# Optimization experiments

Measured on AMD Instinct MI355X. Metric: run time of the kernel, lower is better.

The kernel has to match this reference:

```python
import jax, jax.numpy as jnp
import numpy as np

B, T, C, H = 2, 2048, 1024, 16
HD = C // H
EPS = 1e-5


def _gelu_tanh(x):
    # 0.5*x*(1+tanh(sqrt(2/pi)*(x+0.044715*x^3)))
    c = jnp.sqrt(jnp.asarray(2.0 / np.pi, dtype=x.dtype))
    return 0.5 * x * (1.0 + jnp.tanh(c * (x + 0.044715 * x * x * x)))


def _layernorm(x, g, b):
    mu = jnp.mean(x, axis=-1, keepdims=True)
    var = jnp.mean(jnp.square(x - mu), axis=-1, keepdims=True)
    return (x - mu) * jax.lax.rsqrt(var + EPS) * g + b


def setup_inputs() -> dict:
    key = jax.random.key(0)
    ks = jax.random.split(key, 8)
    s = lambda fan_in: 1.0 / np.sqrt(fan_in)
    return {
        "x": jax.random.normal(ks[0], (B, T, C), jnp.float32),
        "ln1_g": jnp.ones((C,), jnp.float32),
        "ln1_b": jnp.zeros((C,), jnp.float32),
        "W_attn": jax.random.normal(ks[1], (C, 3 * C), jnp.float32) * s(C),
        "b_attn": jnp.zeros((3 * C,), jnp.float32),
        "W_proj": jax.random.normal(ks[2], (C, C), jnp.float32) * s(C),
        "b_proj": jnp.zeros((C,), jnp.float32),
        "ln2_g": jnp.ones((C,), jnp.float32),
        "ln2_b": jnp.zeros((C,), jnp.float32),
        "W_fc": jax.random.normal(ks[3], (C, 4 * C), jnp.float32) * s(C),
        "b_fc": jnp.zeros((4 * C,), jnp.float32),
        "W_fc2": jax.random.normal(ks[4], (4 * C, C), jnp.float32) * s(4 * C),
        "b_fc2": jnp.zeros((C,), jnp.float32),
    }


def reference(x, ln1_g, ln1_b, W_attn, b_attn, W_proj, b_proj,
              ln2_g, ln2_b, W_fc, b_fc, W_fc2, b_fc2):
    # --- attention branch (pre-LN) ---
    h = _layernorm(x, ln1_g, ln1_b)
    qkv = h @ W_attn + b_attn                      # [B,T,3C]
    q, k, v = jnp.split(qkv, 3, axis=2)
    q = q.reshape(B, T, H, HD).transpose(0, 2, 1, 3)  # [B,H,T,HD]
    k = k.reshape(B, T, H, HD).transpose(0, 2, 1, 3)
    v = v.reshape(B, T, H, HD).transpose(0, 2, 1, 3)
    att = jnp.einsum('bhqd,bhkd->bhqk', q, k) / jnp.sqrt(jnp.asarray(HD, x.dtype))
    causal = jnp.tril(jnp.ones((T, T), bool))
    att = jnp.where(causal, att, jnp.asarray(-jnp.inf, att.dtype))
    att = jax.nn.softmax(att, axis=-1)
    y = jnp.einsum('bhqk,bhkd->bhqd', att, v)      # [B,H,T,HD]
    y = y.transpose(0, 2, 1, 3).reshape(B, T, C)
    x = x + (y @ W_proj + b_proj)
    # --- MLP branch (pre-LN) ---
    h = _layernorm(x, ln2_g, ln2_b)
    h = _gelu_tanh(h @ W_fc + b_fc)
    x = x + (h @ W_fc2 + b_fc2)
    return x
```

## Files before the change

### kernel.cpp

```cpp
#include <hip/hip_runtime.h>
#include <hip/hip_bf16.h>
#include <cstdint>
#include <cstddef>

#define B_  2
#define T_  2048
#define C_  1024
#define H_  16
#define HD_ 64
#define M_TOT 4096

typedef __bf16 bf16x8 __attribute__((ext_vector_type(8)));
typedef float  f32x4  __attribute__((ext_vector_type(4)));
typedef unsigned short u16;

__device__ __forceinline__ u16 f2bf(float f) {
  __hip_bfloat16 h = __float2bfloat16(f);
  return __builtin_bit_cast(u16, h);
}

__device__ __forceinline__ void async_cp16(const u16* g, u16* l) {
  __builtin_amdgcn_global_load_lds(
      (const __attribute__((address_space(1))) void*)g,
      (__attribute__((address_space(3))) void*)l, 16, 0, 0);
}

__device__ __forceinline__ float gelu_f(float x) {
  const float z = 0.7978845608028654f * (x + 0.044715f * x * x * x);
  return x / (1.0f + __expf(-2.0f * z));
}

__global__ __launch_bounds__(256) void ln_bf16_kernel(
    const float* __restrict__ x, const float* __restrict__ g,
    const float* __restrict__ b, u16* __restrict__ out) {
  const int row = blockIdx.x;
  const int tid = threadIdx.x;
  const float4 v = reinterpret_cast<const float4*>(x)[row * 256 + tid];
  float s  = v.x + v.y + v.z + v.w;
  float sq = v.x * v.x + v.y * v.y + v.z * v.z + v.w * v.w;
#pragma unroll
  for (int off = 32; off > 0; off >>= 1) {
    s  += __shfl_xor(s, off);
    sq += __shfl_xor(sq, off);
  }
  __shared__ float red[8];
  const int wave = tid >> 6;
  if ((tid & 63) == 0) { red[wave] = s; red[4 + wave] = sq; }
  __syncthreads();
  s  = red[0] + red[1] + red[2] + red[3];
  sq = red[4] + red[5] + red[6] + red[7];
  const float mu   = s * (1.0f / 1024.0f);
  const float rstd = rsqrtf(sq * (1.0f / 1024.0f) - mu * mu + 1e-5f);
  const float4 gv = reinterpret_cast<const float4*>(g)[tid];
  const float4 bv = reinterpret_cast<const float4*>(b)[tid];
  ushort4 o;
  o.x = f2bf((v.x - mu) * rstd * gv.x + bv.x);
  o.y = f2bf((v.y - mu) * rstd * gv.y + bv.y);
  o.z = f2bf((v.z - mu) * rstd * gv.z + bv.z);
  o.w = f2bf((v.w - mu) * rstd * gv.w + bv.w);
  reinterpret_cast<ushort4*>(out)[row * 256 + tid] = o;
}

__global__ __launch_bounds__(256) void transpose_bf16_kernel(
    const float* __restrict__ W, u16* __restrict__ Wt, int K, int N) {
  __shared__ float tile[32][33];
  const int n0 = blockIdx.x * 32, k0 = blockIdx.y * 32;
  const int tx = threadIdx.x & 31;
  const int ty = threadIdx.x >> 5;
#pragma unroll
  for (int i = 0; i < 4; ++i)
    tile[ty + 8 * i][tx] = W[(k0 + ty + 8 * i) * (size_t)N + n0 + tx];
  __syncthreads();
#pragma unroll
  for (int i = 0; i < 4; ++i)
    Wt[(n0 + ty + 8 * i) * (size_t)K + k0 + tx] = f2bf(tile[tx][ty + 8 * i]);
}

template <int MODE, int BM>
__global__ __launch_bounds__(256, 2) void gemm_kernel(
    const u16* __restrict__ A, const u16* __restrict__ Bt,
    const float* __restrict__ bias, const float* __restrict__ resid,
    float* __restrict__ outf, u16* __restrict__ outb,
    u16* __restrict__ qo, u16* __restrict__ ko, u16* __restrict__ vto,
    int M, int N, int K) {
  constexpr int MT = BM / 32;
  __shared__ __align__(16) u16 As[BM * 32];
  __shared__ __align__(16) u16 Bs[128 * 32];
  const int tid  = threadIdx.x;
  const int wave = tid >> 6, lane = tid & 63;
  const int col  = lane & 15, quad = lane >> 4;
  const int wm   = wave >> 1, wn = wave & 1;
  const int bn = blockIdx.x, bm = blockIdx.y;

  const int ar = bm * BM + wave * (BM / 4) + (lane >> 2);
  const int br = bn * 128 + wave * 32 + (lane >> 2);
  const int kc = (lane & 3) * 8;
  const u16* ap = A  + (size_t)ar * K + kc;
  const u16* bp = Bt + (size_t)br * K + kc;
  u16* as_dst = As + wave * (BM / 4) * 32;
  u16* bs_dst = Bs + wave * 1024;

  f32x4 acc[MT][4] = {};

  for (int k0 = 0; k0 < K; k0 += 32) {
    __syncthreads();
    async_cp16(ap + k0, as_dst);
    if constexpr (BM == 128) async_cp16(ap + 16 * K + k0, as_dst + 512);
    async_cp16(bp + k0,          bs_dst);
    async_cp16(bp + 16 * K + k0, bs_dst + 512);
    __syncthreads();
    bf16x8 af[MT], bf[4];
#pragma unroll
    for (int mt = 0; mt < MT; ++mt)
      af[mt] = *reinterpret_cast<const bf16x8*>(&As[(wm * (BM / 2) + mt * 16 + col) * 32 + quad * 8]);
#pragma unroll
    for (int nt = 0; nt < 4; ++nt)
      bf[nt] = *reinterpret_cast<const bf16x8*>(&Bs[(wn * 64 + nt * 16 + col) * 32 + quad * 8]);
#pragma unroll
    for (int mt = 0; mt < MT; ++mt)
#pragma unroll
      for (int nt = 0; nt < 4; ++nt)
        acc[mt][nt] = __builtin_amdgcn_mfma_f32_16x16x32_bf16(af[mt], bf[nt], acc[mt][nt], 0, 0, 0);
  }

#pragma unroll
  for (int mt = 0; mt < MT; ++mt) {
#pragma unroll
    for (int r = 0; r < 4; ++r) {
      const int grow = bm * BM + wm * (BM / 2) + mt * 16 + quad * 4 + r;
#pragma unroll
      for (int nt = 0; nt < 4; ++nt) {
        const int gcol = bn * 128 + wn * 64 + nt * 16 + col;
        const float val = acc[mt][nt][r] + bias[gcol];
        if constexpr (MODE == 0) {
          outb[(size_t)grow * N + gcol] = f2bf(gelu_f(val));
        } else if constexpr (MODE == 1) {
          outf[(size_t)grow * N + gcol] = resid[(size_t)grow * N + gcol] + val;
        } else {
          const int which = gcol >> 10, c = gcol & 1023;
          const int hh = c >> 6, dd = c & 63;
          const int bb = grow >> 11, tt = grow & 2047;
          if (which == 0)
            qo[((bb * H_ + hh) * (size_t)T_ + tt) * HD_ + dd] = f2bf(val * 0.125f);
          else if (which == 1)
            ko[((bb * H_ + hh) * (size_t)T_ + tt) * HD_ + dd] = f2bf(val);
          else
            vto[((bb * H_ + hh) * (size_t)HD_ + dd) * T_ + tt] = f2bf(val);
        }
      }
    }
  }
}

#define PSTR 68
__global__ __launch_bounds__(256, 2) void attn_kernel(
    const u16* __restrict__ q, const u16* __restrict__ k,
    const u16* __restrict__ vt, u16* __restrict__ y) {
  const int bh  = blockIdx.x;
  const int qt  = (T_ / 128 - 1) - blockIdx.y;
  const int tid = threadIdx.x;
  const int wave = tid >> 6, lane = tid & 63;
  const int col = lane & 15, quad = lane >> 4;
  const int b = bh >> 4, h = bh & 15;
  const int r0w = qt * 128 + wave * 32;

  __shared__ __align__(16) u16 Klds[64 * PSTR];
  __shared__ __align__(16) u16 Vtlds[64 * PSTR];
  __shared__ __align__(16) u16 Plds[4 * 32 * PSTR];

  bf16x8 aq[2][2];
#pragma unroll
  for (int i = 0; i < 2; ++i)
#pragma unroll
    for (int j = 0; j < 2; ++j)
      aq[i][j] = *reinterpret_cast<const bf16x8*>(
          &q[((size_t)bh * T_ + r0w + i * 16 + col) * HD_ + j * 32 + quad * 8]);

  bf16x8 ones;
#pragma unroll
  for (int jj = 0; jj < 8; ++jj) ones[jj] = (__bf16)1.0f;

  f32x4 o[2][4] = {};
  f32x4 l_acc[2] = {};

  const int srow = tid >> 3, spart = tid & 7;
  u16* pw = Plds + wave * 32 * PSTR;

  for (int kb = 0; kb <= qt * 128 + 64; kb += 64) {
    __syncthreads();
    *reinterpret_cast<uint4*>(&Klds[srow * PSTR + spart * 8]) =
        *reinterpret_cast<const uint4*>(&k[((size_t)bh * T_ + kb + srow) * HD_ + spart * 8]);
    *reinterpret_cast<uint4*>(&Klds[(srow + 32) * PSTR + spart * 8]) =
        *reinterpret_cast<const uint4*>(&k[((size_t)bh * T_ + kb + srow + 32) * HD_ + spart * 8]);
    *reinterpret_cast<uint4*>(&Vtlds[srow * PSTR + spart * 8]) =
        *reinterpret_cast<const uint4*>(&vt[((size_t)bh * HD_ + srow) * T_ + kb + spart * 8]);
    *reinterpret_cast<uint4*>(&Vtlds[(srow + 32) * PSTR + spart * 8]) =
        *reinterpret_cast<const uint4*>(&vt[((size_t)bh * HD_ + srow + 32) * T_ + kb + spart * 8]);
    __syncthreads();

    if (kb > r0w + 31) continue;

    f32x4 s[2][4];
#pragma unroll
    for (int n = 0; n < 4; ++n) {
      const bf16x8 bk0 = *reinterpret_cast<const bf16x8*>(&Klds[(n * 16 + col) * PSTR + quad * 8]);
      const bf16x8 bk1 = *reinterpret_cast<const bf16x8*>(&Klds[(n * 16 + col) * PSTR + 32 + quad * 8]);
#pragma unroll
      for (int i = 0; i < 2; ++i) {
        f32x4 z = {};
        z = __builtin_amdgcn_mfma_f32_16x16x32_bf16(aq[i][0], bk0, z, 0, 0, 0);
        s[i][n] = __builtin_amdgcn_mfma_f32_16x16x32_bf16(aq[i][1], bk1, z, 0, 0, 0);
      }
    }

    const bool domask = (kb + 63 > r0w);
#pragma unroll
    for (int i = 0; i < 2; ++i) {
#pragma unroll
      for (int n = 0; n < 4; ++n) {
#pragma unroll
        for (int r = 0; r < 4; ++r) {
          float sv = s[i][n][r];
          if (domask) {
            const int key = kb + n * 16 + col;
            const int row = r0w + i * 16 + quad * 4 + r;
            sv = (key <= row) ? sv : -1e30f;
          }
          pw[(i * 16 + quad * 4 + r) * PSTR + n * 16 + col] = f2bf(__expf(sv));
        }
      }
    }
    __builtin_amdgcn_s_waitcnt(0xC07F);

    bf16x8 ap0[2], ap1[2];
#pragma unroll
    for (int i = 0; i < 2; ++i) {
      ap0[i] = *reinterpret_cast<const bf16x8*>(&pw[(i * 16 + col) * PSTR + quad * 8]);
      ap1[i] = *reinterpret_cast<const bf16x8*>(&pw[(i * 16 + col) * PSTR + 32 + quad * 8]);
      l_acc[i] = __builtin_amdgcn_mfma_f32_16x16x32_bf16(ap0[i], ones, l_acc[i], 0, 0, 0);
      l_acc[i] = __builtin_amdgcn_mfma_f32_16x16x32_bf16(ap1[i], ones, l_acc[i], 0, 0, 0);
    }
#pragma unroll
    for (int n = 0; n < 4; ++n) {
      const bf16x8 bv0 = *reinterpret_cast<const bf16x8*>(&Vtlds[(n * 16 + col) * PSTR + quad * 8]);
      const bf16x8 bv1 = *reinterpret_cast<const bf16x8*>(&Vtlds[(n * 16 + col) * PSTR + 32 + quad * 8]);
#pragma unroll
      for (int i = 0; i < 2; ++i) {
        o[i][n] = __builtin_amdgcn_mfma_f32_16x16x32_bf16(ap0[i], bv0, o[i][n], 0, 0, 0);
        o[i][n] = __builtin_amdgcn_mfma_f32_16x16x32_bf16(ap1[i], bv1, o[i][n], 0, 0, 0);
      }
    }
  }

#pragma unroll
  for (int i = 0; i < 2; ++i) {
#pragma unroll
    for (int r = 0; r < 4; ++r) {
      const int qrow = r0w + i * 16 + quad * 4 + r;
      const float inv = 1.0f / l_acc[i][r];
#pragma unroll
      for (int n = 0; n < 4; ++n)
        y[((size_t)b * T_ + qrow) * C_ + h * HD_ + n * 16 + col] = f2bf(o[i][n][r] * inv);
    }
  }
}

extern "C" void kernel_launch(void* const* d_in, const int* in_sizes, int n_in,
                              void* d_out, int out_size, void* d_ws, size_t ws_size,
                              hipStream_t stream) {
  const float* x      = (const float*)d_in[0];
  const float* ln1_g  = (const float*)d_in[1];
  const float* ln1_b  = (const float*)d_in[2];
  const float* W_attn = (const float*)d_in[3];
  const float* b_attn = (const float*)d_in[4];
  const float* W_proj = (const float*)d_in[5];
  const float* b_proj = (const float*)d_in[6];
  const float* ln2_g  = (const float*)d_in[7];
  const float* ln2_b  = (const float*)d_in[8];
  const float* W_fc   = (const float*)d_in[9];
  const float* b_fc   = (const float*)d_in[10];
  const float* W_fc2  = (const float*)d_in[11];
  const float* b_fc2  = (const float*)d_in[12];
  float* out = (float*)d_out;

  char* p = (char*)d_ws;
  auto alloc = [&](size_t bytes) {
    char* r = p;
    p += (bytes + 255) & ~(size_t)255;
    return r;
  };
  u16*   h1      = (u16*)alloc((size_t)M_TOT * C_ * 2);
  u16*   wt_attn = (u16*)alloc((size_t)3 * C_ * C_ * 2);
  u16*   wt_proj = (u16*)alloc((size_t)C_ * C_ * 2);
  u16*   wt_fc   = (u16*)alloc((size_t)4 * C_ * C_ * 2);
  u16*   wt_fc2  = (u16*)alloc((size_t)C_ * 4 * C_ * 2);
  u16*   qbuf    = (u16*)alloc((size_t)M_TOT * C_ * 2);
  u16*   kbuf    = (u16*)alloc((size_t)M_TOT * C_ * 2);
  u16*   vtbuf   = (u16*)alloc((size_t)M_TOT * C_ * 2);
  u16*   ybuf    = (u16*)alloc((size_t)M_TOT * C_ * 2);
  float* x2      = (float*)alloc((size_t)M_TOT * C_ * 4);
  u16*   h2      = (u16*)alloc((size_t)M_TOT * C_ * 2);
  u16*   act     = (u16*)alloc((size_t)M_TOT * 4 * C_ * 2);

  transpose_bf16_kernel<<<dim3(96, 32),  256, 0, stream>>>(W_attn, wt_attn, 1024, 3072);
  transpose_bf16_kernel<<<dim3(32, 32),  256, 0, stream>>>(W_proj, wt_proj, 1024, 1024);
  transpose_bf16_kernel<<<dim3(128, 32), 256, 0, stream>>>(W_fc,   wt_fc,   1024, 4096);
  transpose_bf16_kernel<<<dim3(32, 128), 256, 0, stream>>>(W_fc2,  wt_fc2,  4096, 1024);

  ln_bf16_kernel<<<M_TOT, 256, 0, stream>>>(x, ln1_g, ln1_b, h1);

  gemm_kernel<3, 128><<<dim3(24, 32), 256, 0, stream>>>(h1, wt_attn, b_attn, nullptr,
                                                        nullptr, nullptr, qbuf, kbuf, vtbuf,
                                                        4096, 3072, 1024);
  attn_kernel<<<dim3(32, 16), 256, 0, stream>>>(qbuf, kbuf, vtbuf, ybuf);

  gemm_kernel<1, 64><<<dim3(8, 64), 256, 0, stream>>>(ybuf, wt_proj, b_proj, x,
                                                      x2, nullptr, nullptr, nullptr, nullptr,
                                                      4096, 1024, 1024);
  ln_bf16_kernel<<<M_TOT, 256, 0, stream>>>(x2, ln2_g, ln2_b, h2);

  gemm_kernel<0, 128><<<dim3(32, 32), 256, 0, stream>>>(h2, wt_fc, b_fc, nullptr,
                                                        nullptr, act, nullptr, nullptr, nullptr,
                                                        4096, 4096, 1024);
  gemm_kernel<1, 64><<<dim3(8, 64), 256, 0, stream>>>(act, wt_fc2, b_fc2, x2,
                                                      out, nullptr, nullptr, nullptr, nullptr,
                                                      4096, 1024, 4096);
}
```

Measured before the change: 385.6 us.

## Halve attention query tile and register-prefetch next K/V block

The attention kernel now processes 64 query rows per block (16 per wave) instead of 128, doubling the grid and raising the launch-bounds occupancy hint to 4. It also prefetches the next K/Vt tile into registers while computing on the current LDS tile, replacing the load-then-sync pattern. The aim is more parallelism, less causal-tail imbalance and hidden global-load latency, at the cost of each K/V tile being loaded by twice as many blocks. A redundant duplicate load of kv1 remains in the code.

```diff
diff --git a/kernel.cpp b/kernel.cpp
--- a/kernel.cpp
+++ b/kernel.cpp
@@ -153,115 +153,110 @@
 }
 
 #define PSTR 68
-__global__ __launch_bounds__(256, 2) void attn_kernel(
+__global__ __launch_bounds__(256, 4) void attn_kernel(
     const u16* __restrict__ q, const u16* __restrict__ k,
     const u16* __restrict__ vt, u16* __restrict__ y) {
   const int bh  = blockIdx.x;
-  const int qt  = (T_ / 128 - 1) - blockIdx.y;
+  const int qt  = (T_ / 64 - 1) - blockIdx.y;
   const int tid = threadIdx.x;
   const int wave = tid >> 6, lane = tid & 63;
   const int col = lane & 15, quad = lane >> 4;
   const int b = bh >> 4, h = bh & 15;
-  const int r0w = qt * 128 + wave * 32;
+  const int r0w = qt * 64 + wave * 16;
 
   __shared__ __align__(16) u16 Klds[64 * PSTR];
   __shared__ __align__(16) u16 Vtlds[64 * PSTR];
-  __shared__ __align__(16) u16 Plds[4 * 32 * PSTR];
-
-  bf16x8 aq[2][2];
-#pragma unroll
-  for (int i = 0; i < 2; ++i)
-#pragma unroll
-    for (int j = 0; j < 2; ++j)
-      aq[i][j] = *reinterpret_cast<const bf16x8*>(
-          &q[((size_t)bh * T_ + r0w + i * 16 + col) * HD_ + j * 32 + quad * 8]);
+  __shared__ __align__(16) u16 Plds[4 * 16 * PSTR];
+
+  bf16x8 aq[2];
+#pragma unroll
+  for (int j = 0; j < 2; ++j)
+    aq[j] = *reinterpret_cast<const bf16x8*>(
+        &q[((size_t)bh * T_ + r0w + col) * HD_ + j * 32 + quad * 8]);
 
   bf16x8 ones;
 #pragma unroll
   for (int jj = 0; jj < 8; ++jj) ones[jj] = (__bf16)1.0f;
 
-  f32x4 o[2][4] = {};
-  f32x4 l_acc[2] = {};
+  f32x4 o[4] = {};
+  f32x4 l_acc = {};
 
   const int srow = tid >> 3, spart = tid & 7;
-  u16* pw = Plds + wave * 32 * PSTR;
-
-  for (int kb = 0; kb <= qt * 128 + 64; kb += 64) {
+  u16* pw = Plds + wave * 16 * PSTR;
+  const u16* kbase  = k  + (size_t)bh * T_ * HD_ + srow * HD_ + spart * 8;
+  const u16* vtbase = vt + (size_t)bh * HD_ * T_ + srow * T_ + spart * 8;
+
+  const int kb_last = qt * 64;
+
+  uint4 kv0, kv1, kv2, kv3;
+  kv0 = *reinterpret_cast<const uint4*>(kbase);
+  kv1 = *reinterpret_cast<const uint4*>(kbase + 32 * HD_);
+  kv2 = *reinterpret_cast<const uint4*>(vtbase);
+  kv3 = *reinterpret_cast<const uint4*>(vtbase + 32 * T_);
+
+  for (int kb = 0; kb <= kb_last; kb += 64) {
+    *reinterpret_cast<uint4*>(&Klds[srow * PSTR + spart * 8])        = kv0;
+    *reinterpret_cast<uint4*>(&Klds[(srow + 32) * PSTR + spart * 8]) = kv1;
+    *reinterpret_cast<uint4*>(&Vtlds[srow * PSTR + spart * 8])        = kv2;
+    *reinterpret_cast<uint4*>(&Vtlds[(srow + 32) * PSTR + spart * 8]) = kv3;
     __syncthreads();
-    *reinterpret_cast<uint4*>(&Klds[srow * PSTR + spart * 8]) =
-        *reinterpret_cast<const uint4*>(&k[((size_t)bh * T_ + kb + srow) * HD_ + spart * 8]);
-    *reinterpret_cast<uint4*>(&Klds[(srow + 32) * PSTR + spart * 8]) =
-        *reinterpret_cast<const uint4*>(&k[((size_t)bh * T_ + kb + srow + 32) * HD_ + spart * 8]);
-    *reinterpret_cast<uint4*>(&Vtlds[srow * PSTR + spart * 8]) =
-        *reinterpret_cast<const uint4*>(&vt[((size_t)bh * HD_ + srow) * T_ + kb + spart * 8]);
-    *reinterpret_cast<uint4*>(&Vtlds[(srow + 32) * PSTR + spart * 8]) =
-        *reinterpret_cast<const uint4*>(&vt[((size_t)bh * HD_ + srow + 32) * T_ + kb + spart * 8]);
-    __syncthreads();
-
-    if (kb > r0w + 31) continue;
-
-    f32x4 s[2][4];
+
+    if (kb < kb_last) {
+      const int nk = kb + 64;
+      kv0 = *reinterpret_cast<const uint4*>(kbase + (size_t)nk * HD_);
+      kv1 = *reinterpret_cast<const uint4*>(kbase + (size_t)(nk + 32) * HD_ - 32 * HD_ + 32 * HD_);
+      kv1 = *reinterpret_cast<const uint4*>(kbase + (size_t)nk * HD_ + 32 * HD_);
+      kv2 = *reinterpret_cast<const uint4*>(vtbase + nk);
+      kv3 = *reinterpret_cast<const uint4*>(vtbase + 32 * T_ + nk);
+    }
+
+    f32x4 s[4];
 #pragma unroll
     for (int n = 0; n < 4; ++n) {
       const bf16x8 bk0 = *reinterpret_cast<const bf16x8*>(&Klds[(n * 16 + col) * PSTR + quad * 8]);
       const bf16x8 bk1 = *reinterpret_cast<const bf16x8*>(&Klds[(n * 16 + col) * PSTR + 32 + quad * 8]);
-#pragma unroll
-      for (int i = 0; i < 2; ++i) {
-        f32x4 z = {};
-        z = __builtin_amdgcn_mfma_f32_16x16x32_bf16(aq[i][0], bk0, z, 0, 0, 0);
-        s[i][n] = __builtin_amdgcn_mfma_f32_16x16x32_bf16(aq[i][1], bk1, z, 0, 0, 0);
+      f32x4 z = {};
+      z = __builtin_amdgcn_mfma_f32_16x16x32_bf16(aq[0], bk0, z, 0, 0, 0);
+      s[n] = __builtin_amdgcn_mfma_f32_16x16x32_bf16(aq[1], bk1, z, 0, 0, 0);
+    }
+
+    const bool domask = (kb == kb_last);
+#pragma unroll
+    for (int n = 0; n < 4; ++n) {
+#pragma unroll
+      for (int r = 0; r < 4; ++r) {
+        float sv = s[n][r];
+        if (domask) {
+          const int key = kb + n * 16 + col;
+          const int row = r0w + quad * 4 + r;
+          sv = (key <= row) ? sv : -1e30f;
+        }
+        pw[(quad * 4 + r) * PSTR + n * 16 + col] = f2bf(__expf(sv));
       }
     }
-
-    const bool domask = (kb + 63 > r0w);
-#pragma unroll
-    for (int i = 0; i < 2; ++i) {
-#pragma unroll
-      for (int n = 0; n < 4; ++n) {
-#pragma unroll
-        for (int r = 0; r < 4; ++r) {
-          float sv = s[i][n][r];
-          if (domask) {
-            const int key = kb + n * 16 + col;
-            const int row = r0w + i * 16 + quad * 4 + r;
-            sv = (key <= row) ? sv : -1e30f;
-          }
-          pw[(i * 16 + quad * 4 + r) * PSTR + n * 16 + col] = f2bf(__expf(sv));
-        }
-      }
-    }
     __builtin_amdgcn_s_waitcnt(0xC07F);
 
-    bf16x8 ap0[2], ap1[2];
-#pragma unroll
-    for (int i = 0; i < 2; ++i) {
-      ap0[i] = *reinterpret_cast<const bf16x8*>(&pw[(i * 16 + col) * PSTR + quad * 8]);
-      ap1[i] = *reinterpret_cast<const bf16x8*>(&pw[(i * 16 + col) * PSTR + 32 + quad * 8]);
-      l_acc[i] = __builtin_amdgcn_mfma_f32_16x16x32_bf16(ap0[i], ones, l_acc[i], 0, 0, 0);
-      l_acc[i] = __builtin_amdgcn_mfma_f32_16x16x32_bf16(ap1[i], ones, l_acc[i], 0, 0, 0);
-    }
+    const bf16x8 ap0 = *reinterpret_cast<const bf16x8*>(&pw[col * PSTR + quad * 8]);
+    const bf16x8 ap1 = *reinterpret_cast<const bf16x8*>(&pw[col * PSTR + 32 + quad * 8]);
+    l_acc = __builtin_amdgcn_mfma_f32_16x16x32_bf16(ap0, ones, l_acc, 0, 0, 0);
+    l_acc = __builtin_amdgcn_mfma_f32_16x16x32_bf16(ap1, ones, l_acc, 0, 0, 0);
 #pragma unroll
     for (int n = 0; n < 4; ++n) {
       const bf16x8 bv0 = *reinterpret_cast<const bf16x8*>(&Vtlds[(n * 16 + col) * PSTR + quad * 8]);
       const bf16x8 bv1 = *reinterpret_cast<const bf16x8*>(&Vtlds[(n * 16 + col) * PSTR + 32 + quad * 8]);
-#pragma unroll
-      for (int i = 0; i < 2; ++i) {
-        o[i][n] = __builtin_amdgcn_mfma_f32_16x16x32_bf16(ap0[i], bv0, o[i][n], 0, 0, 0);
-        o[i][n] = __builtin_amdgcn_mfma_f32_16x16x32_bf16(ap1[i], bv1, o[i][n], 0, 0, 0);
-      }
-    }
-  }
-
-#pragma unroll
-  for (int i = 0; i < 2; ++i) {
-#pragma unroll
-    for (int r = 0; r < 4; ++r) {
-      const int qrow = r0w + i * 16 + quad * 4 + r;
-      const float inv = 1.0f / l_acc[i][r];
-#pragma unroll
-      for (int n = 0; n < 4; ++n)
-        y[((size_t)b * T_ + qrow) * C_ + h * HD_ + n * 16 + col] = f2bf(o[i][n][r] * inv);
-    }
+      o[n] = __builtin_amdgcn_mfma_f32_16x16x32_bf16(ap0, bv0, o[n], 0, 0, 0);
+      o[n] = __builtin_amdgcn_mfma_f32_16x16x32_bf16(ap1, bv1, o[n], 0, 0, 0);
+    }
+    __syncthreads();
+  }
+
+#pragma unroll
+  for (int r = 0; r < 4; ++r) {
+    const int qrow = r0w + quad * 4 + r;
+    const float inv = 1.0f / l_acc[r];
+#pragma unroll
+    for (int n = 0; n < 4; ++n)
+      y[((size_t)b * T_ + qrow) * C_ + h * HD_ + n * 16 + col] = f2bf(o[n][r] * inv);
   }
 }
 
@@ -312,7 +307,7 @@
   gemm_kernel<3, 128><<<dim3(24, 32), 256, 0, stream>>>(h1, wt_attn, b_attn, nullptr,
                                                         nullptr, nullptr, qbuf, kbuf, vtbuf,
                                                         4096, 3072, 1024);
-  attn_kernel<<<dim3(32, 16), 256, 0, stream>>>(qbuf, kbuf, vtbuf, ybuf);
+  attn_kernel<<<dim3(32, 32), 256, 0, stream>>>(qbuf, kbuf, vtbuf, ybuf);
 
   gemm_kernel<1, 64><<<dim3(8, 64), 256, 0, stream>>>(ybuf, wt_proj, b_proj, x,
                                                       x2, nullptr, nullptr, nullptr, nullptr,
```

Result: faster. 369.9 us (-4.1%).
